# Performance work log

Measured on AMD Instinct MI355X. Metric: run time of the kernel, lower is better.

## Reference

```python
import jax, jax.numpy as jnp
import numpy as np

N, E, F_IN, H, C = 50000, 800000, 256, 4, 32
NEG_SLOPE_ATT = 0.2   # PyG GATConv default negative_slope for attention LeakyReLU
NEG_SLOPE_ACT = 0.01  # GATLayer's alpha for the post-norm LeakyReLU
EPS = 1e-5            # BatchNorm1d eps


def setup_inputs() -> dict:
    key = jax.random.key(0)
    ks = jax.random.split(key, 8)
    x = jax.random.normal(ks[0], (N, F_IN), jnp.float32)
    edge_idx = jax.random.randint(ks[1], (2, E), 0, N)
    # GATConv params (heads concatenated): lin weight, attention vectors, bias
    W = jax.random.normal(ks[2], (H * C, F_IN), jnp.float32) / np.sqrt(F_IN)
    att_src = jax.random.normal(ks[3], (H, C), jnp.float32) / np.sqrt(C)
    att_dst = jax.random.normal(ks[4], (H, C), jnp.float32) / np.sqrt(C)
    bias = jax.random.normal(ks[5], (H * C,), jnp.float32) * 0.01
    # BatchNorm1d affine params
    gamma = jax.random.normal(ks[6], (H * C,), jnp.float32) * 0.1 + 1.0
    beta = jax.random.normal(ks[7], (H * C,), jnp.float32) * 0.01
    return {"x": x, "edge_idx": edge_idx, "W": W, "att_src": att_src,
            "att_dst": att_dst, "bias": bias, "gamma": gamma, "beta": beta}


def reference(x, edge_idx, W, att_src, att_dst, bias, gamma, beta):
    n = x.shape[0]
    # PyG GATConv adds self-loops by default
    self_loops = jnp.arange(n)
    src = jnp.concatenate([edge_idx[0], self_loops])  # [E+N]
    dst = jnp.concatenate([edge_idx[1], self_loops])

    h = (x @ W.T).reshape(n, H, C)                    # [N, H, C]
    a_s = jnp.einsum('nhc,hc->nh', h, att_src)        # per-node src score
    a_d = jnp.einsum('nhc,hc->nh', h, att_dst)        # per-node dst score

    # edge attention logits, then segment softmax over incoming edges per dst
    e = jax.nn.leaky_relu(a_s[src] + a_d[dst], NEG_SLOPE_ATT)  # [E+N, H]
    e_max = jax.ops.segment_max(e, dst, num_segments=n)
    e_exp = jnp.exp(e - e_max[dst])
    denom = jax.ops.segment_sum(e_exp, dst, num_segments=n)
    alpha = e_exp / denom[dst]                        # [E+N, H]

    # scatter-add aggregation of attended source features
    out = jax.ops.segment_sum(alpha[:, :, None] * h[src], dst, num_segments=n)
    out = out.reshape(n, H * C) + bias                # concat heads + bias

    # BatchNorm1d (training-mode batch statistics) + LeakyReLU(alpha)
    mu = out.mean(axis=0)
    var = out.var(axis=0)
    out = (out - mu) * jax.lax.rsqrt(var + EPS) * gamma + beta
    return jax.nn.leaky_relu(out, NEG_SLOPE_ACT)
```

## Files before the change

kernel.cpp:

```cpp
#include <hip/hip_runtime.h>
#include <hip/hip_bf16.h>
#include <math.h>


typedef __attribute__((ext_vector_type(8))) short bf8_t;
typedef __attribute__((ext_vector_type(4))) float f4_t;

__device__ inline unsigned short f2bf(float f) {
  unsigned u = __float_as_uint(f);
  u += 0x7fff + ((u >> 16) & 1);
  return (unsigned short)(u >> 16);
}
__device__ inline float lrelu02(float v) { return v > 0.f ? v : 0.2f * v; }
__device__ inline float bflo(unsigned g) { return __uint_as_float(g << 16); }
__device__ inline float bfhi(unsigned g) { return __uint_as_float(g & 0xffff0000u); }

#define LSTRIDE 264
#define PSTRIDE 2048
#define SSTRIDE 2112
#define NC 8

__global__ __launch_bounds__(256) void att_fold_k(const float* __restrict__ w,
                                                  const float* __restrict__ att_s,
                                                  const float* __restrict__ att_d,
                                                  float* __restrict__ waug) {
  int j = blockIdx.x;
  int head = j & 3;
  const float* av = (j < 4 ? att_s : att_d) + head * 32;
  int col = threadIdx.x;
  float s = 0.f;
#pragma unroll
  for (int c = 0; c < 32; c++)
    s += av[c] * w[(size_t)(head * 32 + c) * 256 + col];
  waug[j * 256 + col] = s;
}

__global__ __launch_bounds__(256) void gemm_mfma(const float* __restrict__ x,
                                                 const float* __restrict__ w,
                                                 const float* __restrict__ waug,
                                                 unsigned* __restrict__ hb2,
                                                 float* __restrict__ a_s,
                                                 float* __restrict__ a_d,
                                                 int n, int ntiles) {
  __shared__ unsigned short wsl[144 * LSTRIDE];
  __shared__ unsigned short xsl[64 * LSTRIDE];
  int tid = threadIdx.x;
  int lane = tid & 63;
  int wid = tid >> 6;
  int quad = lane >> 4;
  int l15 = lane & 15;

#pragma unroll 4
  for (int i = 0; i < 32; i++) {
    int idx = tid + i * 256;
    int row = idx >> 6;
    int f4 = idx & 63;
    float4 v = *(const float4*)&w[(size_t)row * 256 + f4 * 4];
    unsigned p01 = f2bf(v.x) | ((unsigned)f2bf(v.y) << 16);
    unsigned p23 = f2bf(v.z) | ((unsigned)f2bf(v.w) << 16);
    *(uint2*)&wsl[row * LSTRIDE + f4 * 4] = make_uint2(p01, p23);
  }
#pragma unroll
  for (int i = 0; i < 8; i++) {
    int idx = tid + i * 256;
    int row = idx >> 8;
    int col = idx & 255;
    float v = waug[idx];
    unsigned short hi = f2bf(v);
    float lov = v - __uint_as_float((unsigned)hi << 16);
    wsl[(128 + row) * LSTRIDE + col] = hi;
    wsl[(136 + row) * LSTRIDE + col] = f2bf(lov);
  }

  float4 pre[16];
  int tile = blockIdx.x;
  if (tile < ntiles) {
#pragma unroll
    for (int i = 0; i < 16; i++) {
      int idx = tid + i * 256;
      int row = idx >> 6, f4 = idx & 63;
      int grow = tile * 64 + row;
      pre[i] = (grow < n) ? *(const float4*)&x[(size_t)grow * 256 + f4 * 4]
                          : make_float4(0.f, 0.f, 0.f, 0.f);
    }
  }

  for (; tile < ntiles; tile += gridDim.x) {
    __syncthreads();
#pragma unroll
    for (int i = 0; i < 16; i++) {
      int idx = tid + i * 256;
      int row = idx >> 6, f4 = idx & 63;
      unsigned p01 = f2bf(pre[i].x) | ((unsigned)f2bf(pre[i].y) << 16);
      unsigned p23 = f2bf(pre[i].z) | ((unsigned)f2bf(pre[i].w) << 16);
      *(uint2*)&xsl[row * LSTRIDE + f4 * 4] = make_uint2(p01, p23);
    }
    __syncthreads();

    int nxt = tile + gridDim.x;
    if (nxt < ntiles) {
#pragma unroll
      for (int i = 0; i < 16; i++) {
        int idx = tid + i * 256;
        int row = idx >> 6, f4 = idx & 63;
        int grow = nxt * 64 + row;
        pre[i] = (grow < n) ? *(const float4*)&x[(size_t)grow * 256 + f4 * 4]
                            : make_float4(0.f, 0.f, 0.f, 0.f);
      }
    }

    f4_t acc[9];
#pragma unroll
    for (int t = 0; t < 9; t++) acc[t] = (f4_t){0.f, 0.f, 0.f, 0.f};
    const unsigned short* arow = &xsl[(wid * 16 + l15) * LSTRIDE];
#pragma unroll
    for (int ks = 0; ks < 8; ks++) {
      bf8_t af = *(const bf8_t*)&arow[ks * 32 + quad * 8];
#pragma unroll
      for (int t = 0; t < 9; t++) {
        bf8_t bf = *(const bf8_t*)&wsl[(t * 16 + l15) * LSTRIDE + ks * 32 + quad * 8];
        acc[t] = __builtin_amdgcn_mfma_f32_16x16x32_bf16(af, bf, acc[t], 0, 0, 0);
      }
    }

    int growb = tile * 64 + wid * 16 + quad * 4;
#pragma unroll
    for (int r = 0; r < 4; r++) {
      int grow = growb + r;
      bool ok = grow < n;
      if (ok) {
        unsigned* orow = &hb2[(size_t)grow * 64];
#pragma unroll
        for (int t = 0; t < 4; t++)
          orow[t * 16 + l15] =
              (unsigned)f2bf(acc[t][r]) | ((unsigned)f2bf(acc[t + 4][r]) << 16);
      }
      float v8 = acc[8][r];
      v8 += __shfl_xor(v8, 8, 64);
      if (ok) {
        if (l15 < 4) a_s[grow * 4 + l15] = v8;
        else if (l15 < 8) a_d[grow * 4 + (l15 - 4)] = v8;
      }
    }
  }
}

__global__ __launch_bounds__(1024) void pair_scatter3_k(const int* __restrict__ src,
                                                        const int* __restrict__ dst,
                                                        int* __restrict__ bcnt,
                                                        unsigned* __restrict__ pairs,
                                                        int E, int nb) {
  __shared__ int cnt[1024];
  int t = threadIdx.x;
  int chunk = (E + gridDim.x - 1) / gridDim.x;
  int lo = blockIdx.x * chunk;
  int hi = min(E, lo + chunk);
  for (int i = t; i < nb; i += 1024) cnt[i] = 0;
  __syncthreads();
  for (int i = lo + t; i < hi; i += 1024) atomicAdd(&cnt[dst[i] >> 6], 1);
  __syncthreads();
  for (int i = t; i < nb; i += 1024) {
    int c = cnt[i];
    cnt[i] = c ? atomicAdd(&bcnt[i], c) : 0;
  }
  __syncthreads();
  for (int i = lo + t; i < hi; i += 1024) {
    int d = dst[i];
    int b = d >> 6;
    int pos = atomicAdd(&cnt[b], 1);
    if (pos < PSTRIDE)
      pairs[(size_t)b * PSTRIDE + pos] = (unsigned)src[i] | ((unsigned)(d & 63) << 26);
  }
}

__global__ __launch_bounds__(256) void bucket_csr_k(const unsigned* __restrict__ pairs,
                                                    const int* __restrict__ bcnt,
                                                    int* __restrict__ off,
                                                    int* __restrict__ dlen,
                                                    int* __restrict__ ssrc, int n) {
  __shared__ int hist[64], lofs[64], curs[64];
  int b = blockIdx.x;
  int t = threadIdx.x;
  int d0 = b << 6;
  int dcnt = min(64, n - d0);
  int cnt = min(bcnt[b], PSTRIDE);
  size_t pstart = (size_t)b * PSTRIDE;
  int ob = b * SSTRIDE;
  if (t < 64) hist[t] = (t < dcnt) ? 1 : 0;
  __syncthreads();
  for (int i = t; i < cnt; i += 256) atomicAdd(&hist[pairs[pstart + i] >> 26], 1);
  __syncthreads();
  if (t == 0) {
    int acc = 0;
    for (int k = 0; k < 64; k++) { lofs[k] = acc; acc += hist[k]; }
  }
  __syncthreads();
  if (t < dcnt) {
    int lo = lofs[t];
    off[d0 + t] = ob + lo;
    dlen[d0 + t] = hist[t];
    curs[t] = lo + 1;
    ssrc[ob + lo] = d0 + t;
  }
  __syncthreads();
  for (int i = t; i < cnt; i += 256) {
    unsigned u = pairs[pstart + i];
    int dl = u >> 26;
    int pos = ob + atomicAdd(&curs[dl], 1);
    ssrc[pos] = (int)(u & 0x03FFFFFFu);
  }
}

#define FMA4(g, p)                                                            \
  alo0 = fmaf(p.x, bflo(g.x), alo0); ahi0 = fmaf(p.y, bfhi(g.x), ahi0);       \
  alo1 = fmaf(p.x, bflo(g.y), alo1); ahi1 = fmaf(p.y, bfhi(g.y), ahi1);       \
  alo2 = fmaf(p.x, bflo(g.z), alo2); ahi2 = fmaf(p.y, bfhi(g.z), ahi2);       \
  alo3 = fmaf(p.x, bflo(g.w), alo3); ahi3 = fmaf(p.y, bfhi(g.w), ahi3);

__global__ __launch_bounds__(256) void agg_csr_k(const int* __restrict__ off,
                                                 const int* __restrict__ dlen,
                                                 const int* __restrict__ ssrc,
                                                 const float* __restrict__ a_s,
                                                 const float* __restrict__ a_d,
                                                 const unsigned* __restrict__ hb2,
                                                 float* __restrict__ out,
                                                 float* __restrict__ gstat, int n) {
  __shared__ float lp[4][64 * 4];
  __shared__ int lsrc[4][64];
  __shared__ float bstat[4][256];
  int tid = threadIdx.x;
  int wid = tid >> 6;
  int lane = tid & 63;
  int q = lane >> 4;
  int m = lane & 15;
  int hsel = m >> 3;

  int d = blockIdx.x * 4 + wid;
  bool act = d < n;

  float alo0 = 0.f, alo1 = 0.f, alo2 = 0.f, alo3 = 0.f;
  float ahi0 = 0.f, ahi1 = 0.f, ahi2 = 0.f, ahi3 = 0.f;
  float l0 = 0.f, l1 = 0.f, l2 = 0.f, l3 = 0.f;

  if (act) {
    int start = off[d];
    int end = start + dlen[d];
    float4 ad4 = *(const float4*)&a_d[d * 4];
    for (int base = start; base < end; base += 64) {
      int cnt = min(64, end - base);
      int j = base + lane;
      if (j < end) {
        int s = ssrc[j];
        float4 as4 = *(const float4*)&a_s[s * 4];
        float p0 = __expf(lrelu02(as4.x + ad4.x));
        float p1 = __expf(lrelu02(as4.y + ad4.y));
        float p2 = __expf(lrelu02(as4.z + ad4.z));
        float p3 = __expf(lrelu02(as4.w + ad4.w));
        l0 += p0; l1 += p1; l2 += p2; l3 += p3;
        lsrc[wid][lane] = s;
        *(float4*)&lp[wid][lane * 4] = make_float4(p0, p2, p1, p3);
      }
      int k = 0;
      for (; k + 8 <= cnt; k += 8) {
        int e0 = k + q, e1 = k + 4 + q;
        int s0 = lsrc[wid][e0], s1 = lsrc[wid][e1];
        uint4 g0 = *(const uint4*)&hb2[(size_t)s0 * 64 + m * 4];
        uint4 g1 = *(const uint4*)&hb2[(size_t)s1 * 64 + m * 4];
        float2 p0 = *(const float2*)&lp[wid][e0 * 4 + hsel * 2];
        float2 p1 = *(const float2*)&lp[wid][e1 * 4 + hsel * 2];
        FMA4(g0, p0);
        FMA4(g1, p1);
      }
      for (; k + 4 <= cnt; k += 4) {
        int e0 = k + q;
        int s0 = lsrc[wid][e0];
        uint4 g0 = *(const uint4*)&hb2[(size_t)s0 * 64 + m * 4];
        float2 p0 = *(const float2*)&lp[wid][e0 * 4 + hsel * 2];
        FMA4(g0, p0);
      }
      int rem = cnt - k;
      if (q < rem) {
        int e0 = k + q;
        int s0 = lsrc[wid][e0];
        uint4 g0 = *(const uint4*)&hb2[(size_t)s0 * 64 + m * 4];
        float2 p0 = *(const float2*)&lp[wid][e0 * 4 + hsel * 2];
        FMA4(g0, p0);
      }
    }
  }

#pragma unroll
  for (int o = 16; o < 64; o <<= 1) {
    alo0 += __shfl_xor(alo0, o, 64); alo1 += __shfl_xor(alo1, o, 64);
    alo2 += __shfl_xor(alo2, o, 64); alo3 += __shfl_xor(alo3, o, 64);
    ahi0 += __shfl_xor(ahi0, o, 64); ahi1 += __shfl_xor(ahi1, o, 64);
    ahi2 += __shfl_xor(ahi2, o, 64); ahi3 += __shfl_xor(ahi3, o, 64);
  }
#pragma unroll
  for (int o = 1; o < 64; o <<= 1) {
    l0 += __shfl_xor(l0, o, 64);
    l1 += __shfl_xor(l1, o, 64);
    l2 += __shfl_xor(l2, o, 64);
    l3 += __shfl_xor(l3, o, 64);
  }
  float il_lo = 1.0f / (hsel ? l1 : l0);
  float il_hi = 1.0f / (hsel ? l3 : l2);
  float4 flo = make_float4(0.f, 0.f, 0.f, 0.f);
  float4 fhi = make_float4(0.f, 0.f, 0.f, 0.f);
  if (act) {
    flo = make_float4(alo0 * il_lo, alo1 * il_lo, alo2 * il_lo, alo3 * il_lo);
    fhi = make_float4(ahi0 * il_hi, ahi1 * il_hi, ahi2 * il_hi, ahi3 * il_hi);
  }
  if (q == 0) {
    if (act) {
      *(float4*)&out[(size_t)d * 128 + m * 4] = flo;
      *(float4*)&out[(size_t)d * 128 + 64 + m * 4] = fhi;
    }
    *(float4*)&bstat[wid][m * 4] = flo;
    *(float4*)&bstat[wid][64 + m * 4] = fhi;
    *(float4*)&bstat[wid][128 + m * 4] =
        make_float4(flo.x * flo.x, flo.y * flo.y, flo.z * flo.z, flo.w * flo.w);
    *(float4*)&bstat[wid][192 + m * 4] =
        make_float4(fhi.x * fhi.x, fhi.y * fhi.y, fhi.z * fhi.z, fhi.w * fhi.w);
  }
  __syncthreads();
  float v = bstat[0][tid] + bstat[1][tid] + bstat[2][tid] + bstat[3][tid];
  atomicAdd(&gstat[(blockIdx.x & (NC - 1)) * 256 + tid], v);
}

__global__ __launch_bounds__(256) void bn_apply_k(float* __restrict__ out,
                                                  const float* __restrict__ gstat,
                                                  const float* __restrict__ gamma,
                                                  const float* __restrict__ beta,
                                                  float inv_n, int n4) {
  __shared__ float sc[128], sh[128];
  int tid = threadIdx.x;
  if (tid < 128) {
    float s = 0.f, s2 = 0.f;
#pragma unroll
    for (int c = 0; c < NC; c++) {
      s += gstat[c * 256 + tid];
      s2 += gstat[c * 256 + 128 + tid];
    }
    float mu = s * inv_n;
    float var = s2 * inv_n - mu * mu;
    float rstd = 1.0f / sqrtf(var + 1e-5f);
    float g = gamma[tid] * rstd;
    sc[tid] = g;
    sh[tid] = beta[tid] - mu * g;
  }
  __syncthreads();
  int i = blockIdx.x * 256 + tid;
  if (i >= n4) return;
  float4 v = ((float4*)out)[i];
  int j = (i & 31) << 2;
  const float4 scv = *(const float4*)&sc[j];
  const float4 shv = *(const float4*)&sh[j];
  v.x = fmaf(v.x, scv.x, shv.x);
  v.y = fmaf(v.y, scv.y, shv.y);
  v.z = fmaf(v.z, scv.z, shv.z);
  v.w = fmaf(v.w, scv.w, shv.w);
  v.x = v.x > 0.f ? v.x : 0.01f * v.x;
  v.y = v.y > 0.f ? v.y : 0.01f * v.y;
  v.z = v.z > 0.f ? v.z : 0.01f * v.z;
  v.w = v.w > 0.f ? v.w : 0.01f * v.w;
  ((float4*)out)[i] = v;
}

static inline char* align16(char* p) {
  return (char*)(((uintptr_t)p + 15) & ~(uintptr_t)15);
}

extern "C" void kernel_launch(void* const* d_in, const int* in_sizes, int n_in,
                              void* d_out, int out_size, void* d_ws, size_t ws_size,
                              hipStream_t stream) {
  const float* x     = (const float*)d_in[0];
  const int*   ei    = (const int*)d_in[1];
  const float* W     = (const float*)d_in[2];
  const float* att_s = (const float*)d_in[3];
  const float* att_d = (const float*)d_in[4];
  const float* gamma = (const float*)d_in[6];
  const float* beta  = (const float*)d_in[7];

  int n = in_sizes[0] / 256;
  int E = in_sizes[1] / 2;
  const int* src = ei;
  const int* dstp = ei + E;
  float* out = (float*)d_out;

  int NBUCK = (n + 63) >> 6;
  int ntiles = (n + 63) / 64;

  char* p = (char*)d_ws;
  unsigned* hb2 = (unsigned*)p; p = align16(p + (size_t)n * 64 * 4);
  float* a_s   = (float*)p; p = align16(p + (size_t)n * 4 * 4);
  float* a_d   = (float*)p; p = align16(p + (size_t)n * 4 * 4);
  float* waug  = (float*)p; p = align16(p + 8 * 256 * 4);
  float* gstat = (float*)p;
  int*   bcnt  = (int*)(gstat + NC * 256);
  p = align16((char*)(bcnt + NBUCK));
  int* off     = (int*)p;   p = align16(p + (size_t)n * 4);
  int* dlen    = (int*)p;   p = align16(p + (size_t)n * 4);
  int* ssrc    = (int*)p;   p = align16(p + (size_t)NBUCK * SSTRIDE * 4);
  unsigned* pairs = (unsigned*)p; p = align16(p + (size_t)NBUCK * PSTRIDE * 4);

  hipMemsetAsync(gstat, 0, ((size_t)NC * 256 + NBUCK) * 4, stream);

  att_fold_k<<<8, 256, 0, stream>>>(W, att_s, att_d, waug);
  gemm_mfma<<<256, 256, 0, stream>>>(x, W, waug, hb2, a_s, a_d, n, ntiles);

  pair_scatter3_k<<<64, 1024, 0, stream>>>(src, dstp, bcnt, pairs, E, NBUCK);
  bucket_csr_k<<<NBUCK, 256, 0, stream>>>(pairs, bcnt, off, dlen, ssrc, n);

  agg_csr_k<<<(n + 3) / 4, 256, 0, stream>>>(off, dlen, ssrc, a_s, a_d, hb2, out,
                                             gstat, n);

  bn_apply_k<<<(n * 32 + 255) / 256, 256, 0, stream>>>(out, gstat, gamma, beta,
                                                       1.0f / n, n * 32);
}
```

Baseline: 212.8 us.

## Prefetch gathered rows in aggregation, shuffle sources, precompute BN coefficients

The aggregation kernel now passes source indices between lanes with wave shuffles instead of through LDS. It issues the first feature-row gathers before the attention exp computation and then keeps the main loop software-pipelined, loading the next eight rows while doing the FMAs on the current ones. BatchNorm statistic partials are spread over more atomic slots to reduce contention. The per-channel scale and shift are now computed once in a separate tiny kernel instead of redundantly in every bn_apply block. This costs an extra kernel launch and more registers in the aggregation loop.

```diff
diff --git a/kernel.cpp b/kernel.cpp
--- a/kernel.cpp
+++ b/kernel.cpp
@@ -18,7 +18,7 @@
 #define LSTRIDE 264
 #define PSTRIDE 2048
 #define SSTRIDE 2112
-#define NC 8
+#define NC 32
 
 __global__ __launch_bounds__(256) void att_fold_k(const float* __restrict__ w,
                                                   const float* __restrict__ att_s,
@@ -226,7 +226,6 @@
                                                  float* __restrict__ out,
                                                  float* __restrict__ gstat, int n) {
   __shared__ float lp[4][64 * 4];
-  __shared__ int lsrc[4][64];
   __shared__ float bstat[4][256];
   int tid = threadIdx.x;
   int wid = tid >> 6;
@@ -249,42 +248,57 @@
     for (int base = start; base < end; base += 64) {
       int cnt = min(64, end - base);
       int j = base + lane;
-      if (j < end) {
-        int s = ssrc[j];
-        float4 as4 = *(const float4*)&a_s[s * 4];
-        float p0 = __expf(lrelu02(as4.x + ad4.x));
-        float p1 = __expf(lrelu02(as4.y + ad4.y));
-        float p2 = __expf(lrelu02(as4.z + ad4.z));
-        float p3 = __expf(lrelu02(as4.w + ad4.w));
-        l0 += p0; l1 += p1; l2 += p2; l3 += p3;
-        lsrc[wid][lane] = s;
-        *(float4*)&lp[wid][lane * 4] = make_float4(p0, p2, p1, p3);
-      }
+      int s = ssrc[min(j, end - 1)];
+
+      uint4 g0, g1;
+      bool pipe = (cnt >= 8);
+      if (pipe) {
+        int s0 = __shfl(s, q, 64);
+        int s1 = __shfl(s, 4 + q, 64);
+        g0 = *(const uint4*)&hb2[(size_t)s0 * 64 + m * 4];
+        g1 = *(const uint4*)&hb2[(size_t)s1 * 64 + m * 4];
+      }
+
+      float4 as4 = *(const float4*)&a_s[s * 4];
+      float p0 = __expf(lrelu02(as4.x + ad4.x));
+      float p1 = __expf(lrelu02(as4.y + ad4.y));
+      float p2 = __expf(lrelu02(as4.z + ad4.z));
+      float p3 = __expf(lrelu02(as4.w + ad4.w));
+      if (j < end) { l0 += p0; l1 += p1; l2 += p2; l3 += p3; }
+      *(float4*)&lp[wid][lane * 4] = make_float4(p0, p2, p1, p3);
+
       int k = 0;
-      for (; k + 8 <= cnt; k += 8) {
-        int e0 = k + q, e1 = k + 4 + q;
-        int s0 = lsrc[wid][e0], s1 = lsrc[wid][e1];
-        uint4 g0 = *(const uint4*)&hb2[(size_t)s0 * 64 + m * 4];
-        uint4 g1 = *(const uint4*)&hb2[(size_t)s1 * 64 + m * 4];
-        float2 p0 = *(const float2*)&lp[wid][e0 * 4 + hsel * 2];
-        float2 p1 = *(const float2*)&lp[wid][e1 * 4 + hsel * 2];
-        FMA4(g0, p0);
-        FMA4(g1, p1);
+      for (; k + 16 <= cnt; k += 8) {
+        int s0n = __shfl(s, k + 8 + q, 64);
+        int s1n = __shfl(s, k + 12 + q, 64);
+        uint4 h0 = *(const uint4*)&hb2[(size_t)s0n * 64 + m * 4];
+        uint4 h1 = *(const uint4*)&hb2[(size_t)s1n * 64 + m * 4];
+        float2 pp0 = *(const float2*)&lp[wid][(k + q) * 4 + hsel * 2];
+        float2 pp1 = *(const float2*)&lp[wid][(k + 4 + q) * 4 + hsel * 2];
+        FMA4(g0, pp0);
+        FMA4(g1, pp1);
+        g0 = h0; g1 = h1;
+      }
+      if (pipe) {
+        float2 pp0 = *(const float2*)&lp[wid][(k + q) * 4 + hsel * 2];
+        float2 pp1 = *(const float2*)&lp[wid][(k + 4 + q) * 4 + hsel * 2];
+        FMA4(g0, pp0);
+        FMA4(g1, pp1);
+        k += 8;
       }
       for (; k + 4 <= cnt; k += 4) {
-        int e0 = k + q;
-        int s0 = lsrc[wid][e0];
-        uint4 g0 = *(const uint4*)&hb2[(size_t)s0 * 64 + m * 4];
-        float2 p0 = *(const float2*)&lp[wid][e0 * 4 + hsel * 2];
-        FMA4(g0, p0);
+        int s0 = __shfl(s, k + q, 64);
+        uint4 g = *(const uint4*)&hb2[(size_t)s0 * 64 + m * 4];
+        float2 pp = *(const float2*)&lp[wid][(k + q) * 4 + hsel * 2];
+        FMA4(g, pp);
       }
       int rem = cnt - k;
-      if (q < rem) {
-        int e0 = k + q;
-        int s0 = lsrc[wid][e0];
-        uint4 g0 = *(const uint4*)&hb2[(size_t)s0 * 64 + m * 4];
-        float2 p0 = *(const float2*)&lp[wid][e0 * 4 + hsel * 2];
-        FMA4(g0, p0);
+      if (rem > 0) {
+        int e = min(k + q, cnt - 1);
+        int s0 = __shfl(s, e, 64);
+        uint4 g = *(const uint4*)&hb2[(size_t)s0 * 64 + m * 4];
+        float2 pp = *(const float2*)&lp[wid][e * 4 + hsel * 2];
+        if (q < rem) { FMA4(g, pp); }
       }
     }
   }
@@ -328,26 +342,34 @@
   atomicAdd(&gstat[(blockIdx.x & (NC - 1)) * 256 + tid], v);
 }
 
+__global__ __launch_bounds__(128) void bn_coef_k(const float* __restrict__ gstat,
+                                                 const float* __restrict__ gamma,
+                                                 const float* __restrict__ beta,
+                                                 float* __restrict__ coef,
+                                                 float inv_n) {
+  int tid = threadIdx.x;
+  float s = 0.f, s2 = 0.f;
+#pragma unroll 8
+  for (int c = 0; c < NC; c++) {
+    s += gstat[c * 256 + tid];
+    s2 += gstat[c * 256 + 128 + tid];
+  }
+  float mu = s * inv_n;
+  float var = s2 * inv_n - mu * mu;
+  float rstd = 1.0f / sqrtf(var + 1e-5f);
+  float g = gamma[tid] * rstd;
+  coef[tid] = g;
+  coef[128 + tid] = beta[tid] - mu * g;
+}
+
 __global__ __launch_bounds__(256) void bn_apply_k(float* __restrict__ out,
-                                                  const float* __restrict__ gstat,
-                                                  const float* __restrict__ gamma,
-                                                  const float* __restrict__ beta,
-                                                  float inv_n, int n4) {
+                                                  const float* __restrict__ coef,
+                                                  int n4) {
   __shared__ float sc[128], sh[128];
   int tid = threadIdx.x;
   if (tid < 128) {
-    float s = 0.f, s2 = 0.f;
-#pragma unroll
-    for (int c = 0; c < NC; c++) {
-      s += gstat[c * 256 + tid];
-      s2 += gstat[c * 256 + 128 + tid];
-    }
-    float mu = s * inv_n;
-    float var = s2 * inv_n - mu * mu;
-    float rstd = 1.0f / sqrtf(var + 1e-5f);
-    float g = gamma[tid] * rstd;
-    sc[tid] = g;
-    sh[tid] = beta[tid] - mu * g;
+    sc[tid] = coef[tid];
+    sh[tid] = coef[128 + tid];
   }
   __syncthreads();
   int i = blockIdx.x * 256 + tid;
@@ -397,14 +419,15 @@
   float* a_d   = (float*)p; p = align16(p + (size_t)n * 4 * 4);
   float* waug  = (float*)p; p = align16(p + 8 * 256 * 4);
   float* gstat = (float*)p;
-  int*   bcnt  = (int*)(gstat + NC * 256);
+  float* coef  = gstat + NC * 256;
+  int*   bcnt  = (int*)(coef + 256);
   p = align16((char*)(bcnt + NBUCK));
   int* off     = (int*)p;   p = align16(p + (size_t)n * 4);
   int* dlen    = (int*)p;   p = align16(p + (size_t)n * 4);
   int* ssrc    = (int*)p;   p = align16(p + (size_t)NBUCK * SSTRIDE * 4);
   unsigned* pairs = (unsigned*)p; p = align16(p + (size_t)NBUCK * PSTRIDE * 4);
 
-  hipMemsetAsync(gstat, 0, ((size_t)NC * 256 + NBUCK) * 4, stream);
+  hipMemsetAsync(gstat, 0, ((size_t)NC * 256 + 256 + NBUCK) * 4, stream);
 
   att_fold_k<<<8, 256, 0, stream>>>(W, att_s, att_d, waug);
   gemm_mfma<<<256, 256, 0, stream>>>(x, W, waug, hb2, a_s, a_d, n, ntiles);
@@ -415,6 +438,6 @@
   agg_csr_k<<<(n + 3) / 4, 256, 0, stream>>>(off, dlen, ssrc, a_s, a_d, hb2, out,
                                              gstat, n);
 
-  bn_apply_k<<<(n * 32 + 255) / 256, 256, 0, stream>>>(out, gstat, gamma, beta,
-                                                       1.0f / n, n * 32);
-}
+  bn_coef_k<<<1, 128, 0, stream>>>(gstat, gamma, beta, coef, 1.0f / n);
+  bn_apply_k<<<(n * 32 + 255) / 256, 256, 0, stream>>>(out, coef, n * 32);
+}
```

Result: faster. 203.9 us (-4.2%).
